# Kernel tuning notes

Hardware: AMD Instinct MI355X
Metric: run time of the kernel (lower is better)

Reference implementation:

```python
import jax, jax.numpy as jnp
import numpy as np

H = 12          # num_attention_heads
D = 64          # num_embed_hidden == attention_head_size
B, T = 4, 2048
SCALE = 1.0 / np.sqrt(D)


def setup_inputs() -> dict:
    key = jax.random.key(0)
    ks = jax.random.split(key, 7)
    P = H * D  # num_attn_proj = 768
    s = 1.0 / np.sqrt(D)
    return {
        "hidden_states": jax.random.normal(ks[0], (B, T, D), dtype=jnp.float32),
        "attention_mask": jnp.ones((B, T), dtype=jnp.float32),
        "Wq": jax.random.normal(ks[1], (D, P), dtype=jnp.float32) * s,
        "bq": jnp.zeros((P,), dtype=jnp.float32),
        "Wk": jax.random.normal(ks[2], (D, P), dtype=jnp.float32) * s,
        "bk": jnp.zeros((P,), dtype=jnp.float32),
        "Wv": jax.random.normal(ks[3], (D, P), dtype=jnp.float32) * s,
        "bv": jnp.zeros((P,), dtype=jnp.float32),
    }


def reference(hidden_states, attention_mask, Wq, bq, Wk, bk, Wv, bv):
    b, t, _ = hidden_states.shape
    # QKV projections -> [B, H, T, D]
    def proj(W, bias):
        return (hidden_states @ W + bias).reshape(b, t, H, D).transpose(0, 2, 1, 3)
    q = proj(Wq, bq)
    k = proj(Wk, bk)
    v = proj(Wv, bv)
    # [B, H, T, T] scores
    scores = jnp.einsum("bhqd,bhkd->bhqk", q, k) * SCALE
    mask = (1.0 - attention_mask)[:, None, None, :] * -10000.0
    scores = scores + mask
    attn = jax.nn.softmax(scores, axis=-1)
    # dropout is identity in eval mode
    y = jnp.einsum("bhqk,bhkd->bhqd", attn, v)
    return y.transpose(0, 2, 1, 3).reshape(b, t, H * D)
```

## Files before the change

### kernel.cpp

```cpp
#include <hip/hip_runtime.h>
#include <hip/hip_bf16.h>

#define NH 12
#define HD 64
#define NB 4
#define SEQ 2048
#define NP 768
#define LOG2E 1.44269504f
#define MASK_L2 14426.9504f

typedef __bf16 bf16x8 __attribute__((ext_vector_type(8)));
typedef __bf16 bf16x2 __attribute__((ext_vector_type(2)));
typedef float f32x2 __attribute__((ext_vector_type(2)));
typedef float f32x4 __attribute__((ext_vector_type(4)));
typedef float f32x16 __attribute__((ext_vector_type(16)));
typedef unsigned u32x4 __attribute__((ext_vector_type(4)));

static __device__ __forceinline__ bf16x8 load_bf16x8(const __bf16* p) {
    return *reinterpret_cast<const bf16x8*>(p);
}
static __device__ __forceinline__ float hw_exp2(float x) {
    return __builtin_amdgcn_exp2f(x);
}
static __device__ __forceinline__ unsigned cvtpk2(float lo, float hi) {
    f32x2 t; t[0] = lo; t[1] = hi;
    return __builtin_bit_cast(unsigned, __builtin_convertvector(t, bf16x2));
}
static __device__ __forceinline__ void async16(const __bf16* g, __bf16* l) {
    __builtin_amdgcn_global_load_lds(
        (const __attribute__((address_space(1))) unsigned*)(g),
        (__attribute__((address_space(3))) unsigned*)(l), 16, 0, 0);
}

__global__ __launch_bounds__(256) void qkv_kernel(
    const float* __restrict__ hidden,
    const float* __restrict__ Wq, const float* __restrict__ Wk,
    const float* __restrict__ Wv,
    const float* __restrict__ bq, const float* __restrict__ bk,
    const float* __restrict__ bv,
    __bf16* __restrict__ Qw, __bf16* __restrict__ Kf, __bf16* __restrict__ Vf)
{
    __shared__ __bf16 wtileT[64][72];
    __shared__ __bf16 ot[64][72];

    const int tid  = threadIdx.x;
    const int lane = tid & 63;
    const int w    = tid >> 6;
    const int g    = lane >> 4;
    const int n    = lane & 15;
    const int n32  = lane & 31;
    const int hi   = lane >> 5;

    const int row0 = blockIdx.x * 64;
    const int gi   = blockIdx.y;
    const int b_   = row0 >> 11;
    const int t0   = row0 & (SEQ - 1);
    const int kb64 = t0 >> 6;

    const float* hrow = hidden + (size_t)(row0 + w * 16 + n) * HD + 8 * g;
    f32x4 h0 = *(const f32x4*)(hrow);
    f32x4 h1 = *(const f32x4*)(hrow + 4);
    f32x4 h2 = *(const f32x4*)(hrow + 32);
    f32x4 h3 = *(const f32x4*)(hrow + 36);
    bf16x8 a0, a1;
    #pragma unroll
    for (int j = 0; j < 4; ++j) {
        a0[j]     = (__bf16)h0[j];
        a0[j + 4] = (__bf16)h1[j];
        a1[j]     = (__bf16)h2[j];
        a1[j + 4] = (__bf16)h3[j];
    }

    const int dr   = tid >> 2;
    const int coff = (tid & 3) * 16;

    for (int tt = 0; tt < 6; ++tt) {
        const int tile_id = gi * 6 + tt;
        const int proj    = tile_id / 12;
        const int head    = tile_id % 12;
        const int bh      = b_ * NH + head;
        const float* W    = proj == 0 ? Wq : (proj == 1 ? Wk : Wv);
        const float* bias = proj == 0 ? bq : (proj == 1 ? bk : bv);
        const float qs    = (proj == 0) ? 0.125f * LOG2E : 1.0f;

        const float* wr = W + (size_t)dr * NP + head * 64 + coff;
        f32x4 x0 = *(const f32x4*)(wr);
        f32x4 x1 = *(const f32x4*)(wr + 4);
        f32x4 x2 = *(const f32x4*)(wr + 8);
        f32x4 x3 = *(const f32x4*)(wr + 12);
        #pragma unroll
        for (int i = 0; i < 4; ++i) {
            wtileT[coff + i     ][dr] = (__bf16)(x0[i] * qs);
            wtileT[coff + 4 + i ][dr] = (__bf16)(x1[i] * qs);
            wtileT[coff + 8 + i ][dr] = (__bf16)(x2[i] * qs);
            wtileT[coff + 12 + i][dr] = (__bf16)(x3[i] * qs);
        }
        __syncthreads();

        #pragma unroll
        for (int dt = 0; dt < 4; ++dt) {
            const bf16x8 b0 = *(const bf16x8*)&wtileT[dt * 16 + n][8 * g];
            const bf16x8 b1 = *(const bf16x8*)&wtileT[dt * 16 + n][32 + 8 * g];
            f32x4 acc = {0.f, 0.f, 0.f, 0.f};
            acc = __builtin_amdgcn_mfma_f32_16x16x32_bf16(a0, b0, acc, 0, 0, 0);
            acc = __builtin_amdgcn_mfma_f32_16x16x32_bf16(a1, b1, acc, 0, 0, 0);
            const float bb = bias[head * 64 + dt * 16 + n] * qs;
            #pragma unroll
            for (int r = 0; r < 4; ++r)
                ot[w * 16 + 4 * g + r][dt * 16 + n] = (__bf16)(acc[r] + bb);
        }
        __syncthreads();

        if (proj == 0) {
            __bf16* dst = Qw + ((size_t)bh * SEQ + t0 + w * 16) * HD;
            const int tr = lane >> 2;
            const int d0 = (lane & 3) * 16;
            *(bf16x8*)(dst + (size_t)tr * HD + d0)     = *(const bf16x8*)&ot[w * 16 + tr][d0];
            *(bf16x8*)(dst + (size_t)tr * HD + d0 + 8) = *(const bf16x8*)&ot[w * 16 + tr][d0 + 8];
        } else if (proj == 1) {
            __bf16* base = Kf + (size_t)bh * SEQ * HD + (size_t)kb64 * 4096;
            #pragma unroll
            for (int sub = 0; sub < 2; ++sub) {
                const bf16x8 fr = *(const bf16x8*)&ot[sub * 32 + n32][w * 16 + 8 * hi];
                *(bf16x8*)(base + (size_t)(w * 2 + sub) * 512 + lane * 8) = fr;
            }
        } else {
            __bf16* base = Vf + (size_t)bh * SEQ * HD + (size_t)kb64 * 4096;
            #pragma unroll
            for (int dsub = 0; dsub < 2; ++dsub) {
                bf16x8 v;
                #pragma unroll
                for (int j = 0; j < 8; ++j)
                    v[j] = ot[w * 16 + ((j & 3) + 8 * (j >> 2) + 4 * hi)][dsub * 32 + n32];
                *(bf16x8*)(base + (size_t)(w * 2 + dsub) * 512 + lane * 8) = v;
            }
        }
    }
}

struct KVbuf {
    __bf16 k[2][4096];
    __bf16 v[3][4096];
};

union FlashLds {
    KVbuf s;
    float et[4][32][68];
};

static __device__ __forceinline__ int rot3(int x) { return x + 1 == 3 ? 0 : x + 1; }

template<int KS, bool STG, bool DOPV>
static __device__ __forceinline__ void fbody(
    int t, int vprev, int vnext, int w, int lane, int n32,
    FlashLds* u, const __bf16* mdd, const __bf16* gsrc,
    const bf16x8 (&qf)[4], const bf16x8& qone,
    f32x16& sap, f32x16& sbp, f32x16& san, f32x16& sbn,
    f32x16& o0, f32x16& o1, f32x2& lsl2)
{
    if (STG) {
        __bf16* dst = (w < 2) ? &u->s.k[KS ^ 1][0] + (w & 1) * 2048
                              : &u->s.v[vnext][0] + (w & 1) * 2048;
        const __bf16* src = gsrc + (size_t)(t + 1) * 4096;
        #pragma unroll
        for (int c = 0; c < 4; ++c) async16(src + c * 512, dst + c * 512);
    }

    const __bf16* Kb = &u->s.k[KS][0];
    bf16x8 kca[4], kcb[4];
    #pragma unroll
    for (int d = 0; d < 4; ++d) {
        kca[d] = load_bf16x8(Kb + (2 * d) * 512 + lane * 8);
        kcb[d] = load_bf16x8(Kb + (2 * d + 1) * 512 + lane * 8);
    }
    const int kb = t << 6;
    bf16x8 maa, mab;
    #pragma unroll
    for (int j = 0; j < 8; ++j) { maa[j] = (__bf16)0.0f; mab[j] = (__bf16)0.0f; }
    maa[0] = mdd[kb + n32];
    mab[0] = mdd[kb + 32 + n32];

    f32x16 z = {0,0,0,0,0,0,0,0,0,0,0,0,0,0,0,0};
    san = z; sbn = z;
    __builtin_amdgcn_s_setprio(1);
    #pragma unroll
    for (int d = 0; d < 4; ++d)
        san = __builtin_amdgcn_mfma_f32_32x32x16_bf16(kca[d], qf[d], san, 0, 0, 0);
    san = __builtin_amdgcn_mfma_f32_32x32x16_bf16(maa, qone, san, 0, 0, 0);
    #pragma unroll
    for (int d = 0; d < 4; ++d)
        sbn = __builtin_amdgcn_mfma_f32_32x32x16_bf16(kcb[d], qf[d], sbn, 0, 0, 0);
    sbn = __builtin_amdgcn_mfma_f32_32x32x16_bf16(mab, qone, sbn, 0, 0, 0);
    __builtin_amdgcn_s_setprio(0);

    if (DOPV) {
        const __bf16* Vb = &u->s.v[vprev][0];
        bf16x8 P0, P1;
        {
            u32x4 B0, B1;
            #pragma unroll
            for (int i = 0; i < 4; ++i) {
                float e0 = hw_exp2(sap[2 * i]),     e1 = hw_exp2(sap[2 * i + 1]);
                float f0 = hw_exp2(sap[8 + 2 * i]), f1 = hw_exp2(sap[8 + 2 * i + 1]);
                B0[i] = cvtpk2(e0, e1);
                B1[i] = cvtpk2(f0, f1);
                f32x2 acc; acc[0] = e0 + f0; acc[1] = e1 + f1;
                lsl2 += acc;
            }
            P0 = __builtin_bit_cast(bf16x8, B0);
            P1 = __builtin_bit_cast(bf16x8, B1);
        }
        {
            bf16x8 v0 = load_bf16x8(Vb + 0 * 512 + lane * 8);
            bf16x8 v1 = load_bf16x8(Vb + 1 * 512 + lane * 8);
            bf16x8 v2 = load_bf16x8(Vb + 2 * 512 + lane * 8);
            bf16x8 v3 = load_bf16x8(Vb + 3 * 512 + lane * 8);
            __builtin_amdgcn_s_setprio(1);
            o0 = __builtin_amdgcn_mfma_f32_32x32x16_bf16(v0, P0, o0, 0, 0, 0);
            o1 = __builtin_amdgcn_mfma_f32_32x32x16_bf16(v1, P0, o1, 0, 0, 0);
            o0 = __builtin_amdgcn_mfma_f32_32x32x16_bf16(v2, P1, o0, 0, 0, 0);
            o1 = __builtin_amdgcn_mfma_f32_32x32x16_bf16(v3, P1, o1, 0, 0, 0);
            __builtin_amdgcn_s_setprio(0);
        }
        bf16x8 P2, P3;
        {
            u32x4 B0, B1;
            #pragma unroll
            for (int i = 0; i < 4; ++i) {
                float e0 = hw_exp2(sbp[2 * i]),     e1 = hw_exp2(sbp[2 * i + 1]);
                float f0 = hw_exp2(sbp[8 + 2 * i]), f1 = hw_exp2(sbp[8 + 2 * i + 1]);
                B0[i] = cvtpk2(e0, e1);
                B1[i] = cvtpk2(f0, f1);
                f32x2 acc; acc[0] = e0 + f0; acc[1] = e1 + f1;
                lsl2 += acc;
            }
            P2 = __builtin_bit_cast(bf16x8, B0);
            P3 = __builtin_bit_cast(bf16x8, B1);
        }
        {
            bf16x8 v4 = load_bf16x8(Vb + 4 * 512 + lane * 8);
            bf16x8 v5 = load_bf16x8(Vb + 5 * 512 + lane * 8);
            bf16x8 v6 = load_bf16x8(Vb + 6 * 512 + lane * 8);
            bf16x8 v7 = load_bf16x8(Vb + 7 * 512 + lane * 8);
            __builtin_amdgcn_s_setprio(1);
            o0 = __builtin_amdgcn_mfma_f32_32x32x16_bf16(v4, P2, o0, 0, 0, 0);
            o1 = __builtin_amdgcn_mfma_f32_32x32x16_bf16(v5, P2, o1, 0, 0, 0);
            o0 = __builtin_amdgcn_mfma_f32_32x32x16_bf16(v6, P3, o0, 0, 0, 0);
            o1 = __builtin_amdgcn_mfma_f32_32x32x16_bf16(v7, P3, o1, 0, 0, 0);
            __builtin_amdgcn_s_setprio(0);
        }
    }
    __syncthreads();
}

__global__ __launch_bounds__(256, 3) void flash_attn_kernel(
    const __bf16* __restrict__ Qw, const __bf16* __restrict__ Kf,
    const __bf16* __restrict__ Vf, const float* __restrict__ amask,
    float* __restrict__ out)
{
    __shared__ __align__(16) FlashLds u;
    __shared__ __bf16 mdd[SEQ];

    const int tid  = threadIdx.x;
    const int lane = tid & 63;
    const int w    = tid >> 6;
    const int n32  = lane & 31;
    const int hi   = lane >> 5;

    const int bid  = blockIdx.x;
    const int xcd  = bid & 7;
    const int slot = bid >> 3;
    const int bh   = xcd * 6 + (slot >> 4);
    const int qblk = slot & 15;
    const int b_   = bh / NH;
    const int h    = bh % NH;
    const int q0   = qblk * 128 + w * 32;

    const float* mp = amask + (size_t)b_ * SEQ;
    #pragma unroll
    for (int i = 0; i < 8; ++i) {
        const int idx = w * 512 + i * 64 + lane;
        mdd[idx] = (__bf16)fmaf(mp[idx], MASK_L2, -MASK_L2);
    }

    const __bf16* Qrow = Qw + ((size_t)bh * SEQ + q0 + n32) * HD + 8 * hi;
    bf16x8 qf[4];
    #pragma unroll
    for (int d = 0; d < 4; ++d) qf[d] = load_bf16x8(Qrow + d * 16);

    bf16x8 qone;
    #pragma unroll
    for (int j = 0; j < 8; ++j) qone[j] = (__bf16)0.0f;
    if (hi == 0) qone[0] = (__bf16)1.0f;

    const size_t bhoff = (size_t)bh * SEQ * HD;
    const __bf16* gsrc = (w < 2 ? Kf : Vf) + bhoff + (w & 1) * 2048 + (size_t)lane * 8;

    {
        __bf16* dst = (w < 2) ? &u.s.k[0][0] + (w & 1) * 2048
                              : &u.s.v[0][0] + (w & 1) * 2048;
        #pragma unroll
        for (int c = 0; c < 4; ++c) async16(gsrc + c * 512, dst + c * 512);
    }
    __syncthreads();

    f32x16 o0 = {0,0,0,0,0,0,0,0,0,0,0,0,0,0,0,0};
    f32x16 o1 = {0,0,0,0,0,0,0,0,0,0,0,0,0,0,0,0};
    f32x2 lsl2 = {0.f, 0.f};
    f32x16 saA, sbA, saB, sbB;

    fbody<0, true, false>(0, 0, 1, w, lane, n32, &u, mdd, gsrc,
                          qf, qone, saA, sbA, saA, sbA, o0, o1, lsl2);

    int vprev = 0, vnext = 2;
    #pragma unroll 1
    for (int tp = 0; tp < 15; ++tp) {
        const int t = 2 * tp + 1;
        fbody<1, true, true>(t, vprev, vnext, w, lane, n32, &u, mdd, gsrc,
                             qf, qone, saA, sbA, saB, sbB, o0, o1, lsl2);
        vprev = rot3(vprev); vnext = rot3(vnext);
        fbody<0, true, true>(t + 1, vprev, vnext, w, lane, n32, &u, mdd, gsrc,
                             qf, qone, saB, sbB, saA, sbA, o0, o1, lsl2);
        vprev = rot3(vprev); vnext = rot3(vnext);
    }
    fbody<1, false, true>(31, vprev, 0, w, lane, n32, &u, mdd, gsrc,
                          qf, qone, saA, sbA, saB, sbB, o0, o1, lsl2);

    {
        const __bf16* Vb = &u.s.v[1][0];
        bf16x8 P0, P1, P2, P3;
        {
            u32x4 B0, B1;
            #pragma unroll
            for (int i = 0; i < 4; ++i) {
                float e0 = hw_exp2(saB[2 * i]),     e1 = hw_exp2(saB[2 * i + 1]);
                float f0 = hw_exp2(saB[8 + 2 * i]), f1 = hw_exp2(saB[8 + 2 * i + 1]);
                B0[i] = cvtpk2(e0, e1); B1[i] = cvtpk2(f0, f1);
                f32x2 acc; acc[0] = e0 + f0; acc[1] = e1 + f1;
                lsl2 += acc;
            }
            P0 = __builtin_bit_cast(bf16x8, B0);
            P1 = __builtin_bit_cast(bf16x8, B1);
        }
        {
            u32x4 B0, B1;
            #pragma unroll
            for (int i = 0; i < 4; ++i) {
                float e0 = hw_exp2(sbB[2 * i]),     e1 = hw_exp2(sbB[2 * i + 1]);
                float f0 = hw_exp2(sbB[8 + 2 * i]), f1 = hw_exp2(sbB[8 + 2 * i + 1]);
                B0[i] = cvtpk2(e0, e1); B1[i] = cvtpk2(f0, f1);
                f32x2 acc; acc[0] = e0 + f0; acc[1] = e1 + f1;
                lsl2 += acc;
            }
            P2 = __builtin_bit_cast(bf16x8, B0);
            P3 = __builtin_bit_cast(bf16x8, B1);
        }
        #pragma unroll
        for (int c = 0; c < 4; ++c) {
            bf16x8 va = load_bf16x8(Vb + (2 * c) * 512 + lane * 8);
            bf16x8 vb = load_bf16x8(Vb + (2 * c + 1) * 512 + lane * 8);
            const bf16x8 P = c == 0 ? P0 : (c == 1 ? P1 : (c == 2 ? P2 : P3));
            o0 = __builtin_amdgcn_mfma_f32_32x32x16_bf16(va, P, o0, 0, 0, 0);
            o1 = __builtin_amdgcn_mfma_f32_32x32x16_bf16(vb, P, o1, 0, 0, 0);
        }
    }

    float rs = lsl2[0] + lsl2[1];
    rs += __shfl_xor(rs, 32);

    __syncthreads();

    #pragma unroll
    for (int k = 0; k < 4; ++k) {
        f32x4 t0, t1;
        #pragma unroll
        for (int j = 0; j < 4; ++j) { t0[j] = o0[4 * k + j]; t1[j] = o1[4 * k + j]; }
        *(f32x4*)&u.et[w][n32][8 * k + 4 * hi]      = t0;
        *(f32x4*)&u.et[w][n32][32 + 8 * k + 4 * hi] = t1;
    }
    const int d0 = (lane & 7) * 8;
    #pragma unroll
    for (int pass = 0; pass < 4; ++pass) {
        const int q = pass * 8 + (lane >> 3);
        const float linv = 1.0f / __shfl(rs, q);
        const float* er = &u.et[w][q][d0];
        f32x4 r0 = *(const f32x4*)(er);
        f32x4 r1 = *(const f32x4*)(er + 4);
        #pragma unroll
        for (int i = 0; i < 4; ++i) { r0[i] *= linv; r1[i] *= linv; }
        float* orow = out + ((size_t)b_ * SEQ + q0 + q) * NP + h * HD + d0;
        *(f32x4*)(orow)     = r0;
        *(f32x4*)(orow + 4) = r1;
    }
}

extern "C" void kernel_launch(void* const* d_in, const int* in_sizes, int n_in,
                              void* d_out, int out_size, void* d_ws, size_t ws_size,
                              hipStream_t stream) {
    const float* hidden = (const float*)d_in[0];
    const float* amask  = (const float*)d_in[1];
    const float* Wq     = (const float*)d_in[2];
    const float* bq     = (const float*)d_in[3];
    const float* Wk     = (const float*)d_in[4];
    const float* bk     = (const float*)d_in[5];
    const float* Wv     = (const float*)d_in[6];
    const float* bv     = (const float*)d_in[7];
    float* out = (float*)d_out;

    const size_t elems = (size_t)NB * NH * SEQ * HD;
    __bf16* Qw = (__bf16*)d_ws;
    __bf16* Kf = Qw + elems;
    __bf16* Vf = Kf + elems;

    qkv_kernel<<<dim3(128, 6), 256, 0, stream>>>(
        hidden, Wq, Wk, Wv, bq, bk, bv, Qw, Kf, Vf);

    flash_attn_kernel<<<dim3(768), 256, 0, stream>>>(
        Qw, Kf, Vf, amask, out);
}
```

Measured before the change: 156.1 us.

## Pre-transpose weights in separate kernel, double-buffer qkv output tile, drop setprio

Adds a small wprep kernel that converts the Q/K/V weights to transposed, pre-scaled bf16 in workspace, along with the scaled biases. The qkv kernel then reads its B fragments straight from global memory and no longer does a per-tile LDS transpose and barrier. Its output tile is double-buffered so one sync per iteration is enough. It also removes the s_setprio hints around the MFMA blocks in the flash kernel. The cost is one extra kernel launch and scattered global reads of B fragments.

```diff
diff --git a/kernel.cpp b/kernel.cpp
--- a/kernel.cpp
+++ b/kernel.cpp
@@ -32,16 +32,43 @@
         (__attribute__((address_space(3))) unsigned*)(l), 16, 0, 0);
 }
 
-__global__ __launch_bounds__(256) void qkv_kernel(
-    const float* __restrict__ hidden,
+__global__ __launch_bounds__(256) void wprep_kernel(
     const float* __restrict__ Wq, const float* __restrict__ Wk,
     const float* __restrict__ Wv,
     const float* __restrict__ bq, const float* __restrict__ bk,
     const float* __restrict__ bv,
+    __bf16* __restrict__ Wt, float* __restrict__ bt)
+{
+    const int blk  = blockIdx.x;
+    const int proj = blk / 12;
+    const int pb   = blk % 12;
+    const float* W    = proj == 0 ? Wq : (proj == 1 ? Wk : Wv);
+    const float* bias = proj == 0 ? bq : (proj == 1 ? bk : bv);
+    const float qs    = (proj == 0) ? 0.125f * LOG2E : 1.0f;
+
+    const int t  = threadIdx.x;
+    const int p  = pb * 64 + (t >> 2);
+    const int kc = (t & 3) * 16;
+
+    bf16x8 o0, o1;
+    #pragma unroll
+    for (int i = 0; i < 8; ++i) {
+        o0[i] = (__bf16)(W[(size_t)(kc + i) * NP + p] * qs);
+        o1[i] = (__bf16)(W[(size_t)(kc + 8 + i) * NP + p] * qs);
+    }
+    __bf16* dst = Wt + ((size_t)proj * NP + p) * 64 + kc;
+    *(bf16x8*)(dst)     = o0;
+    *(bf16x8*)(dst + 8) = o1;
+
+    if (t < 64) bt[proj * NP + pb * 64 + t] = bias[pb * 64 + t] * qs;
+}
+
+__global__ __launch_bounds__(256) void qkv_kernel(
+    const float* __restrict__ hidden,
+    const __bf16* __restrict__ Wt, const float* __restrict__ bt,
     __bf16* __restrict__ Qw, __bf16* __restrict__ Kf, __bf16* __restrict__ Vf)
 {
-    __shared__ __bf16 wtileT[64][72];
-    __shared__ __bf16 ot[64][72];
+    __shared__ __bf16 ot[2][64][72];
 
     const int tid  = threadIdx.x;
     const int lane = tid & 63;
@@ -71,43 +98,28 @@
         a1[j + 4] = (__bf16)h3[j];
     }
 
-    const int dr   = tid >> 2;
-    const int coff = (tid & 3) * 16;
-
     for (int tt = 0; tt < 6; ++tt) {
         const int tile_id = gi * 6 + tt;
         const int proj    = tile_id / 12;
         const int head    = tile_id % 12;
         const int bh      = b_ * NH + head;
-        const float* W    = proj == 0 ? Wq : (proj == 1 ? Wk : Wv);
-        const float* bias = proj == 0 ? bq : (proj == 1 ? bk : bv);
-        const float qs    = (proj == 0) ? 0.125f * LOG2E : 1.0f;
-
-        const float* wr = W + (size_t)dr * NP + head * 64 + coff;
-        f32x4 x0 = *(const f32x4*)(wr);
-        f32x4 x1 = *(const f32x4*)(wr + 4);
-        f32x4 x2 = *(const f32x4*)(wr + 8);
-        f32x4 x3 = *(const f32x4*)(wr + 12);
-        #pragma unroll
-        for (int i = 0; i < 4; ++i) {
-            wtileT[coff + i     ][dr] = (__bf16)(x0[i] * qs);
-            wtileT[coff + 4 + i ][dr] = (__bf16)(x1[i] * qs);
-            wtileT[coff + 8 + i ][dr] = (__bf16)(x2[i] * qs);
-            wtileT[coff + 12 + i][dr] = (__bf16)(x3[i] * qs);
-        }
-        __syncthreads();
+
+        const __bf16* wp = Wt + ((size_t)proj * NP + head * 64) * 64;
+        const float*  bp = bt + proj * NP + head * 64;
+        auto& otb = ot[tt & 1];
 
         #pragma unroll
         for (int dt = 0; dt < 4; ++dt) {
-            const bf16x8 b0 = *(const bf16x8*)&wtileT[dt * 16 + n][8 * g];
-            const bf16x8 b1 = *(const bf16x8*)&wtileT[dt * 16 + n][32 + 8 * g];
+            const __bf16* wrow = wp + (size_t)(dt * 16 + n) * 64;
+            const bf16x8 b0 = load_bf16x8(wrow + 8 * g);
+            const bf16x8 b1 = load_bf16x8(wrow + 32 + 8 * g);
             f32x4 acc = {0.f, 0.f, 0.f, 0.f};
             acc = __builtin_amdgcn_mfma_f32_16x16x32_bf16(a0, b0, acc, 0, 0, 0);
             acc = __builtin_amdgcn_mfma_f32_16x16x32_bf16(a1, b1, acc, 0, 0, 0);
-            const float bb = bias[head * 64 + dt * 16 + n] * qs;
+            const float bb = bp[dt * 16 + n];
             #pragma unroll
             for (int r = 0; r < 4; ++r)
-                ot[w * 16 + 4 * g + r][dt * 16 + n] = (__bf16)(acc[r] + bb);
+                otb[w * 16 + 4 * g + r][dt * 16 + n] = (__bf16)(acc[r] + bb);
         }
         __syncthreads();
 
@@ -115,13 +127,13 @@
             __bf16* dst = Qw + ((size_t)bh * SEQ + t0 + w * 16) * HD;
             const int tr = lane >> 2;
             const int d0 = (lane & 3) * 16;
-            *(bf16x8*)(dst + (size_t)tr * HD + d0)     = *(const bf16x8*)&ot[w * 16 + tr][d0];
-            *(bf16x8*)(dst + (size_t)tr * HD + d0 + 8) = *(const bf16x8*)&ot[w * 16 + tr][d0 + 8];
+            *(bf16x8*)(dst + (size_t)tr * HD + d0)     = *(const bf16x8*)&otb[w * 16 + tr][d0];
+            *(bf16x8*)(dst + (size_t)tr * HD + d0 + 8) = *(const bf16x8*)&otb[w * 16 + tr][d0 + 8];
         } else if (proj == 1) {
             __bf16* base = Kf + (size_t)bh * SEQ * HD + (size_t)kb64 * 4096;
             #pragma unroll
             for (int sub = 0; sub < 2; ++sub) {
-                const bf16x8 fr = *(const bf16x8*)&ot[sub * 32 + n32][w * 16 + 8 * hi];
+                const bf16x8 fr = *(const bf16x8*)&otb[sub * 32 + n32][w * 16 + 8 * hi];
                 *(bf16x8*)(base + (size_t)(w * 2 + sub) * 512 + lane * 8) = fr;
             }
         } else {
@@ -131,7 +143,7 @@
                 bf16x8 v;
                 #pragma unroll
                 for (int j = 0; j < 8; ++j)
-                    v[j] = ot[w * 16 + ((j & 3) + 8 * (j >> 2) + 4 * hi)][dsub * 32 + n32];
+                    v[j] = otb[w * 16 + ((j & 3) + 8 * (j >> 2) + 4 * hi)][dsub * 32 + n32];
                 *(bf16x8*)(base + (size_t)(w * 2 + dsub) * 512 + lane * 8) = v;
             }
         }
@@ -182,7 +194,6 @@
 
     f32x16 z = {0,0,0,0,0,0,0,0,0,0,0,0,0,0,0,0};
     san = z; sbn = z;
-    __builtin_amdgcn_s_setprio(1);
     #pragma unroll
     for (int d = 0; d < 4; ++d)
         san = __builtin_amdgcn_mfma_f32_32x32x16_bf16(kca[d], qf[d], san, 0, 0, 0);
@@ -191,7 +202,6 @@
     for (int d = 0; d < 4; ++d)
         sbn = __builtin_amdgcn_mfma_f32_32x32x16_bf16(kcb[d], qf[d], sbn, 0, 0, 0);
     sbn = __builtin_amdgcn_mfma_f32_32x32x16_bf16(mab, qone, sbn, 0, 0, 0);
-    __builtin_amdgcn_s_setprio(0);
 
     if (DOPV) {
         const __bf16* Vb = &u->s.v[vprev][0];
@@ -215,12 +225,10 @@
             bf16x8 v1 = load_bf16x8(Vb + 1 * 512 + lane * 8);
             bf16x8 v2 = load_bf16x8(Vb + 2 * 512 + lane * 8);
             bf16x8 v3 = load_bf16x8(Vb + 3 * 512 + lane * 8);
-            __builtin_amdgcn_s_setprio(1);
             o0 = __builtin_amdgcn_mfma_f32_32x32x16_bf16(v0, P0, o0, 0, 0, 0);
             o1 = __builtin_amdgcn_mfma_f32_32x32x16_bf16(v1, P0, o1, 0, 0, 0);
             o0 = __builtin_amdgcn_mfma_f32_32x32x16_bf16(v2, P1, o0, 0, 0, 0);
             o1 = __builtin_amdgcn_mfma_f32_32x32x16_bf16(v3, P1, o1, 0, 0, 0);
-            __builtin_amdgcn_s_setprio(0);
         }
         bf16x8 P2, P3;
         {
@@ -242,12 +250,10 @@
             bf16x8 v5 = load_bf16x8(Vb + 5 * 512 + lane * 8);
             bf16x8 v6 = load_bf16x8(Vb + 6 * 512 + lane * 8);
             bf16x8 v7 = load_bf16x8(Vb + 7 * 512 + lane * 8);
-            __builtin_amdgcn_s_setprio(1);
             o0 = __builtin_amdgcn_mfma_f32_32x32x16_bf16(v4, P2, o0, 0, 0, 0);
             o1 = __builtin_amdgcn_mfma_f32_32x32x16_bf16(v5, P2, o1, 0, 0, 0);
             o0 = __builtin_amdgcn_mfma_f32_32x32x16_bf16(v6, P3, o0, 0, 0, 0);
             o1 = __builtin_amdgcn_mfma_f32_32x32x16_bf16(v7, P3, o1, 0, 0, 0);
-            __builtin_amdgcn_s_setprio(0);
         }
     }
     __syncthreads();
@@ -411,9 +417,12 @@
     __bf16* Qw = (__bf16*)d_ws;
     __bf16* Kf = Qw + elems;
     __bf16* Vf = Kf + elems;
-
-    qkv_kernel<<<dim3(128, 6), 256, 0, stream>>>(
-        hidden, Wq, Wk, Wv, bq, bk, bv, Qw, Kf, Vf);
+    __bf16* Wt = Vf + elems;
+    float*  bt = (float*)(Wt + (size_t)3 * NP * 64);
+
+    wprep_kernel<<<dim3(36), 256, 0, stream>>>(Wq, Wk, Wv, bq, bk, bv, Wt, bt);
+
+    qkv_kernel<<<dim3(128, 6), 256, 0, stream>>>(hidden, Wt, bt, Qw, Kf, Vf);
 
     flash_attn_kernel<<<dim3(768), 256, 0, stream>>>(
         Qw, Kf, Vf, amask, out);
```

After: 165.0 us. 5.7% more time.
